# Kernel tuning notes

Hardware: AMD Instinct MI355X
Metric: run time of the kernel (lower is better)

## Reference

```python
import jax, jax.numpy as jnp
import numpy as np

B, S, H = 4, 128, 768
OUT, TAG = 24, 4


def setup_inputs() -> dict:
    key = jax.random.key(0)
    k1, k2, k3, k4, k5 = jax.random.split(key, 5)
    x = jax.random.normal(k1, (B, S, H), dtype=jnp.float32)
    # linear1: in 2H -> out 3H ; linear2: in 3H -> out TAG*OUT
    s1 = 1.0 / np.sqrt(2 * H)
    s2 = 1.0 / np.sqrt(3 * H)
    W1 = jax.random.uniform(k2, (2 * H, 3 * H), minval=-s1, maxval=s1, dtype=jnp.float32)
    b1 = jax.random.uniform(k3, (3 * H,), minval=-s1, maxval=s1, dtype=jnp.float32)
    W2 = jax.random.uniform(k4, (3 * H, TAG * OUT), minval=-s2, maxval=s2, dtype=jnp.float32)
    b2 = jax.random.uniform(k5, (TAG * OUT,), minval=-s2, maxval=s2, dtype=jnp.float32)
    return {"x": x, "W1": W1, "b1": b1, "W2": W2, "b2": b2}


def reference(x, W1, b1, W2, b2):
    b, s, h = x.shape
    # pairs[b,i,j] = concat(x[b,i], x[b,j]); avoid explicit 2H concat by
    # splitting W1 into head/tail halves (same math as cat -> linear1).
    W1h, W1t = W1[:h], W1[h:]
    head = jnp.einsum('bih,hk->bik', x, W1h)          # [B,S,3H]
    tail = jnp.einsum('bjh,hk->bjk', x, W1t)          # [B,S,3H]
    hid = head[:, :, None, :] + tail[:, None, :, :] + b1  # [B,S,S,3H]
    hid = jax.nn.relu(hid)  # dropout is identity in eval mode
    scores = jnp.einsum('bijk,ko->bijo', hid, W2) + b2     # [B,S,S,TAG*OUT]
    return scores.reshape(b, s, s, OUT, TAG)
```

## Files before the change

### kernel.cpp

```cpp
#include <hip/hip_runtime.h>
#include <hip/hip_bf16.h>


typedef __bf16 bf16x8 __attribute__((ext_vector_type(8)));
typedef _Float16 f16x8 __attribute__((ext_vector_type(8)));
typedef float f32x4 __attribute__((ext_vector_type(4)));

#define S_   128
#define H_   768
#define K3   2304
#define NOUT 96
#define NIT  36

__device__ __forceinline__ unsigned short f2bf(float f) {
    union { __bf16 b; unsigned short u; } c;
    c.b = (__bf16)f;
    return c.u;
}

__device__ __forceinline__ unsigned short f2h(float f) {
    union { _Float16 h; unsigned short u; } c;
    c.h = (_Float16)f;
    return c.u;
}

__device__ __forceinline__ void gload_lds16(const unsigned short* g, unsigned short* l) {
    __builtin_amdgcn_global_load_lds(
        (const __attribute__((address_space(1))) void*)g,
        (__attribute__((address_space(3))) void*)l,
        16, 0, 0);
}

__global__ __launch_bounds__(256) void k_prep(
        const float* __restrict__ x, unsigned short* __restrict__ xb,
        const float* __restrict__ W1, unsigned short* __restrict__ w1t,
        const float* __restrict__ W2, unsigned short* __restrict__ w2f) {
    __shared__ float tile[32][33];
    const int bid = blockIdx.x, tid = threadIdx.x;
    if (bid < 384) {
        int t = bid * 256 + tid;
        float4 v = ((const float4*)x)[t];
        ushort4 o;
        o.x = f2bf(v.x); o.y = f2bf(v.y); o.z = f2bf(v.z); o.w = f2bf(v.w);
        ((ushort4*)xb)[t] = o;
    } else if (bid < 3840) {
        int idx = bid - 384;
        int bx = idx % 72, by = (idx / 72) % 24, bz = idx / 1728;
        const float* src = W1 + (size_t)bz * H_ * K3;
        unsigned short* dst = w1t + (size_t)bz * K3 * H_;
        int c0 = bx * 32, r0 = by * 32;
        int row = tid >> 3, c4 = (tid & 7) * 4;
        float4 v = *(const float4*)(src + (size_t)(r0 + row) * K3 + c0 + c4);
        tile[row][c4 + 0] = v.x; tile[row][c4 + 1] = v.y;
        tile[row][c4 + 2] = v.z; tile[row][c4 + 3] = v.w;
        __syncthreads();
        ushort4 o;
        o.x = f2bf(tile[c4 + 0][row]); o.y = f2bf(tile[c4 + 1][row]);
        o.z = f2bf(tile[c4 + 2][row]); o.w = f2bf(tile[c4 + 3][row]);
        *(ushort4*)(dst + (size_t)(c0 + row) * H_ + r0 + c4) = o;
    } else {
        int t = (bid - 3840) * 256 + tid;
        int l = t & 63, f = (t >> 6) % 6, kc = t / 384;
        int k0 = kc * 32 + (l >> 4) * 8;
        int o  = f * 16 + (l & 15);
        unsigned short v[8];
#pragma unroll
        for (int e = 0; e < 8; e++)
            v[e] = f2h(W2[(size_t)(k0 + e) * NOUT + o]);
        *(uint4*)(w2f + (size_t)t * 8) = *(const uint4*)v;
    }
}

__global__ __launch_bounds__(256) void k_gemm1(
        const unsigned short* __restrict__ xb,
        const unsigned short* __restrict__ w1t,
        const float* __restrict__ b1,
        unsigned short* __restrict__ headh,
        unsigned short* __restrict__ tailsw) {
    __shared__ __align__(16) unsigned short AB[3][6144];
    const int tid = threadIdx.x;
    const int l = tid & 63, w = tid >> 6;
    const int m0 = blockIdx.y * 64;
    const int n0 = blockIdx.x * 128;
    const int wr = (w >> 1) * 32, wc = (w & 1) * 64;
    const int lr = l & 15, lk = (l >> 4) * 8;
    f32x4 acc[2][4] = {};
    const int NKT = H_ / 32;

    auto stage = [&](int sbuf, int kt) {
        {
            int row = tid >> 2, seg = (tid & 3) * 8;
            gload_lds16(xb + (size_t)(m0 + row) * H_ + kt * 32 + seg, &AB[sbuf][tid * 8]);
        }
#pragma unroll
        for (int p = 0; p < 2; ++p) {
            int idx = p * 256 + tid;
            int row = idx >> 2, seg = (idx & 3) * 8;
            gload_lds16(w1t + (size_t)(n0 + row) * H_ + kt * 32 + seg,
                        &AB[sbuf][2048 + idx * 8]);
        }
    };

    stage(0, 0);
    stage(1, 1);

    for (int n = 0; n < NKT; ++n) {
        asm volatile("s_waitcnt vmcnt(3)" ::: "memory");
        __builtin_amdgcn_s_barrier();
        stage((n + 2) % 3, (n + 2 < NKT) ? (n + 2) : (NKT - 1));

        const unsigned short* Ab = &AB[n % 3][0];
        const unsigned short* Bb = &AB[n % 3][2048];
        bf16x8 af[2], bfr[4];
#pragma unroll
        for (int i = 0; i < 2; i++) af[i]  = *(const bf16x8*)(Ab + (wr + i * 16 + lr) * 32 + lk);
#pragma unroll
        for (int j = 0; j < 4; j++) bfr[j] = *(const bf16x8*)(Bb + (wc + j * 16 + lr) * 32 + lk);
#pragma unroll
        for (int i = 0; i < 2; i++)
#pragma unroll
            for (int j = 0; j < 4; j++)
                acc[i][j] = __builtin_amdgcn_mfma_f32_16x16x32_bf16(af[i], bfr[j], acc[i][j], 0, 0, 0);
    }

    const bool tailblk = (n0 >= K3);
    const int nloc = n0 - (tailblk ? K3 : 0);
    const int lv = (l >> 4) * 4;
    if (!tailblk) {
#pragma unroll
        for (int j = 0; j < 4; j++) {
            int c = nloc + wc + j * 16 + lr;
#pragma unroll
            for (int i = 0; i < 2; i++) {
                int mrow = m0 + wr + i * 16 + lv;
#pragma unroll
                for (int e = 0; e < 4; e++)
                    headh[(size_t)(mrow + e) * K3 + c] = f2h(acc[i][j][e]);
            }
        }
    } else {
#pragma unroll
        for (int j = 0; j < 4; j++) {
            int c = nloc + wc + j * 16 + lr;
            float bias = b1[c];
            int chunk = c >> 6, kin = c & 63, u = kin >> 3, ee = kin & 7;
#pragma unroll
            for (int i = 0; i < 2; i++) {
                int mrow = m0 + wr + i * 16 + lv;
#pragma unroll
                for (int e = 0; e < 4; e++) {
                    int r = mrow + e;
                    int jbg = r >> 4, rr = r & 15;
                    size_t idx = (((size_t)(jbg * 36 + chunk) * 8 + u) * 16 + rr) * 8 + ee;
                    tailsw[idx] = f2h(acc[i][j][e] + bias);
                }
            }
        }
    }
}

__device__ __forceinline__ f16x8 form8t(uint4 hq, f16x8 t) {
    union { uint4 q; f16x8 v; } H;
    H.q = hq;
    f16x8 s = H.v + t;
    const f16x8 z = {0, 0, 0, 0, 0, 0, 0, 0};
    return __builtin_elementwise_max(s, z);
}

__global__ __launch_bounds__(256) void k_pair(
        const unsigned short* __restrict__ headh,
        const unsigned short* __restrict__ tailsw,
        const unsigned short* __restrict__ w2f,
        const float* __restrict__ b2,
        float* __restrict__ out) {
    __shared__ __align__(16) unsigned short wlds[4][6144];
    __shared__ __align__(16) unsigned short tlds[4][1024];

    const int tid = threadIdx.x;
    const int w = tid >> 6, l = tid & 63;
    const int lr = l & 15, lkq = l >> 4;
    const int lkoff = lkq * 8;
    const int jb = blockIdx.x;
    const int ig = blockIdx.y;
    const int b  = blockIdx.z;
    const int i0 = ig * 8;

    {
        int bid = jb + ig * 8 + b * 128;
        if ((bid >> 8) & 1) {
            __builtin_amdgcn_s_sleep(11);
            __builtin_amdgcn_s_sleep(11);
        }
    }

    const unsigned short* Hp   = headh + (size_t)(b * S_ + i0 + 2 * w) * K3;
    const unsigned short* Tsrc = tailsw + (size_t)(b * 8 + jb) * 36 * 1024;

    f32x4 acc[2][6] = {};
    float b2v[6];
#pragma unroll
    for (int f = 0; f < 6; f++) b2v[f] = b2[f * 16 + lr];

    auto stage = [&](int sbuf, int c) {
        const unsigned short* wsrc = w2f + (size_t)c * 6144;
#pragma unroll
        for (int i = 0; i < 3; ++i)
            gload_lds16(wsrc + i * 2048 + tid * 8, &wlds[sbuf][i * 2048 + tid * 8]);
        const unsigned short* tsrc = Tsrc + (size_t)c * 1024;
#pragma unroll
        for (int h = 0; h < 2; ++h)
            gload_lds16(tsrc + h * 512 + l * 8, &tlds[sbuf][h * 512 + l * 8]);
    };

    stage(0, 0);
    stage(1, 1);
    uint4 ha[2], hb[2];
#pragma unroll
    for (int kk = 0; kk < 2; kk++) {
        ha[kk] = *(const uint4*)(Hp + kk * 32 + lkoff);
        hb[kk] = *(const uint4*)(Hp + K3 + kk * 32 + lkoff);
    }

    for (int n = 0; n < NIT; ++n) {
        stage((n + 2) & 3, (n + 2 < NIT) ? (n + 2) : (NIT - 1));
        const int kn = ((n < NIT - 1) ? (n + 1) : n) * 64;
        uint4 han[2], hbn[2];
#pragma unroll
        for (int kk = 0; kk < 2; kk++) {
            han[kk] = *(const uint4*)(Hp + kn + kk * 32 + lkoff);
            hbn[kk] = *(const uint4*)(Hp + K3 + kn + kk * 32 + lkoff);
        }

        asm volatile("s_waitcnt vmcnt(9)" ::: "memory");
        __builtin_amdgcn_s_barrier();

        const unsigned short* Lb = &wlds[n & 3][0];
        const unsigned short* Tb = &tlds[n & 3][0];
        __builtin_amdgcn_s_setprio(1);
#pragma unroll
        for (int kk = 0; kk < 2; kk++) {
            f16x8 t8 = *(const f16x8*)(Tb + (kk * 4 + lkq) * 128 + lr * 8);
            f16x8 a0 = form8t(ha[kk], t8);
            f16x8 a1 = form8t(hb[kk], t8);
#pragma unroll
            for (int f = 0; f < 6; f++) {
                f16x8 bfr = *(const f16x8*)(Lb + kk * 3072 + f * 512 + l * 8);
                acc[0][f] = __builtin_amdgcn_mfma_f32_16x16x32_f16(a0, bfr, acc[0][f], 0, 0, 0);
                acc[1][f] = __builtin_amdgcn_mfma_f32_16x16x32_f16(a1, bfr, acc[1][f], 0, 0, 0);
            }
        }
        __builtin_amdgcn_s_setprio(0);
#pragma unroll
        for (int kk = 0; kk < 2; kk++) { ha[kk] = han[kk]; hb[kk] = hbn[kk]; }
    }

    float* O = out + (((size_t)(b * S_ + i0 + 2 * w)) * S_ + jb * 16) * NOUT;
#pragma unroll
    for (int q = 0; q < 2; q++)
#pragma unroll
        for (int f = 0; f < 6; f++)
#pragma unroll
            for (int e = 0; e < 4; e++) {
                int j = lkq * 4 + e;
                O[(size_t)q * S_ * NOUT + (size_t)j * NOUT + f * 16 + lr] = acc[q][f][e] + b2v[f];
            }
}

extern "C" void kernel_launch(void* const* d_in, const int* in_sizes, int n_in,
                              void* d_out, int out_size, void* d_ws, size_t ws_size,
                              hipStream_t stream) {
    const float* x  = (const float*)d_in[0];
    const float* W1 = (const float*)d_in[1];
    const float* b1 = (const float*)d_in[2];
    const float* W2 = (const float*)d_in[3];
    const float* b2 = (const float*)d_in[4];
    float* out = (float*)d_out;

    char* ws = (char*)d_ws;
    unsigned short* xb     = (unsigned short*)(ws);
    unsigned short* w1t    = (unsigned short*)(ws +   786432);
    unsigned short* w2f    = (unsigned short*)(ws +  7864320);
    unsigned short* headh  = (unsigned short*)(ws +  8306688);
    unsigned short* tailsw = (unsigned short*)(ws + 10665984);

    hipLaunchKernelGGL(k_prep, dim3(3948), dim3(256), 0, stream,
                       x, xb, W1, w1t, W2, w2f);
    hipLaunchKernelGGL(k_gemm1, dim3(36, 8), dim3(256), 0, stream,
                       xb, w1t, b1, headh, tailsw);
    hipLaunchKernelGGL(k_pair, dim3(8, 16, 4), dim3(256), 0, stream,
                       headh, tailsw, w2f, b2, out);
}
```

Measured before the change: 58.55 us.

## Switch pair kernel to 32x32 MFMA tiles with split-K across wave groups

Moves the pair kernel from 16x16x32 to 32x32x16 MFMA. The W2 and tail layouts written by the prep and gemm1 kernels change to match. Each block now covers 32 j-columns and 4 i-rows. Its two wave groups each handle half of the K range, and the partial sums are reduced through LDS at the end. Staging drops to a 3-buffer ring per group issued after the barrier, and the s_sleep staggering is removed. The aim is higher MFMA efficiency and more reuse per fragment, at the cost of an extra LDS reduction and half the waves idling during the epilogue.

```diff
diff --git a/kernel.cpp b/kernel.cpp
--- a/kernel.cpp
+++ b/kernel.cpp
@@ -5,12 +5,13 @@
 typedef __bf16 bf16x8 __attribute__((ext_vector_type(8)));
 typedef _Float16 f16x8 __attribute__((ext_vector_type(8)));
 typedef float f32x4 __attribute__((ext_vector_type(4)));
+typedef float f32x16 __attribute__((ext_vector_type(16)));
 
 #define S_   128
 #define H_   768
 #define K3   2304
 #define NOUT 96
-#define NIT  36
+#define NITG 36
 
 __device__ __forceinline__ unsigned short f2bf(float f) {
     union { __bf16 b; unsigned short u; } c;
@@ -60,9 +61,9 @@
         *(ushort4*)(dst + (size_t)(c0 + row) * H_ + r0 + c4) = o;
     } else {
         int t = (bid - 3840) * 256 + tid;
-        int l = t & 63, f = (t >> 6) % 6, kc = t / 384;
-        int k0 = kc * 32 + (l >> 4) * 8;
-        int o  = f * 16 + (l & 15);
+        int l = t & 63, og = (t >> 6) % 3, s = t / 192;
+        int k0 = s * 16 + (l >> 5) * 8;
+        int o  = og * 32 + (l & 31);
         unsigned short v[8];
 #pragma unroll
         for (int e = 0; e < 8; e++)
@@ -143,15 +144,15 @@
         for (int j = 0; j < 4; j++) {
             int c = nloc + wc + j * 16 + lr;
             float bias = b1[c];
-            int chunk = c >> 6, kin = c & 63, u = kin >> 3, ee = kin & 7;
+            int chunk = c >> 5, kin = c & 31, u = kin >> 3, ee = kin & 7;
 #pragma unroll
             for (int i = 0; i < 2; i++) {
                 int mrow = m0 + wr + i * 16 + lv;
 #pragma unroll
                 for (int e = 0; e < 4; e++) {
                     int r = mrow + e;
-                    int jbg = r >> 4, rr = r & 15;
-                    size_t idx = (((size_t)(jbg * 36 + chunk) * 8 + u) * 16 + rr) * 8 + ee;
+                    int jbg = r >> 5, rr = r & 31;
+                    size_t idx = (((size_t)(jbg * 72 + chunk) * 4 + u) * 32 + rr) * 8 + ee;
                     tailsw[idx] = f2h(acc[i][j][e] + bias);
                 }
             }
@@ -173,97 +174,125 @@
         const unsigned short* __restrict__ w2f,
         const float* __restrict__ b2,
         float* __restrict__ out) {
-    __shared__ __align__(16) unsigned short wlds[4][6144];
-    __shared__ __align__(16) unsigned short tlds[4][1024];
+    __shared__ __align__(16) unsigned short smem[24576];
 
     const int tid = threadIdx.x;
     const int w = tid >> 6, l = tid & 63;
-    const int lr = l & 15, lkq = l >> 4;
-    const int lkoff = lkq * 8;
+    const int g  = w >> 1;
+    const int wi = w & 1;
+    const int p  = w & 1;
+    const int lo = l & 31;
+    const int kq = l >> 5;
+    const int ko = kq * 8;
     const int jb = blockIdx.x;
     const int ig = blockIdx.y;
     const int b  = blockIdx.z;
-    const int i0 = ig * 8;
-
-    {
-        int bid = jb + ig * 8 + b * 128;
-        if ((bid >> 8) & 1) {
-            __builtin_amdgcn_s_sleep(11);
-            __builtin_amdgcn_s_sleep(11);
-        }
-    }
-
-    const unsigned short* Hp   = headh + (size_t)(b * S_ + i0 + 2 * w) * K3;
-    const unsigned short* Tsrc = tailsw + (size_t)(b * 8 + jb) * 36 * 1024;
-
-    f32x4 acc[2][6] = {};
-    float b2v[6];
-#pragma unroll
-    for (int f = 0; f < 6; f++) b2v[f] = b2[f * 16 + lr];
-
-    auto stage = [&](int sbuf, int c) {
-        const unsigned short* wsrc = w2f + (size_t)c * 6144;
+    const int i0 = ig * 4 + wi * 2;
+    const int cbase = g * NITG;
+
+    const unsigned short* Hp   = headh + (size_t)(b * S_ + i0) * K3;
+    const unsigned short* Tsrc = tailsw + (size_t)(b * 4 + jb) * 72 * 1024;
+
+    f32x16 acc[2][3] = {};
+
+    auto stage = [&](int sbuf, int n) {
+        const int cc = g * NITG + n;
+        const unsigned short* wsrc = w2f + (size_t)cc * 3072;
+        unsigned short* wdst = &smem[(g * 3 + sbuf) * 3072];
 #pragma unroll
         for (int i = 0; i < 3; ++i)
-            gload_lds16(wsrc + i * 2048 + tid * 8, &wlds[sbuf][i * 2048 + tid * 8]);
-        const unsigned short* tsrc = Tsrc + (size_t)c * 1024;
-#pragma unroll
-        for (int h = 0; h < 2; ++h)
-            gload_lds16(tsrc + h * 512 + l * 8, &tlds[sbuf][h * 512 + l * 8]);
+            gload_lds16(wsrc + (p * 3 + i) * 512 + l * 8, wdst + (p * 3 + i) * 512 + l * 8);
+        const unsigned short* tsrc = Tsrc + (size_t)cc * 1024;
+        unsigned short* tdst = &smem[18432 + (g * 3 + sbuf) * 1024];
+        gload_lds16(tsrc + p * 512 + l * 8, tdst + p * 512 + l * 8);
     };
 
     stage(0, 0);
     stage(1, 1);
-    uint4 ha[2], hb[2];
-#pragma unroll
-    for (int kk = 0; kk < 2; kk++) {
-        ha[kk] = *(const uint4*)(Hp + kk * 32 + lkoff);
-        hb[kk] = *(const uint4*)(Hp + K3 + kk * 32 + lkoff);
-    }
-
-    for (int n = 0; n < NIT; ++n) {
-        stage((n + 2) & 3, (n + 2 < NIT) ? (n + 2) : (NIT - 1));
-        const int kn = ((n < NIT - 1) ? (n + 1) : n) * 64;
-        uint4 han[2], hbn[2];
-#pragma unroll
-        for (int kk = 0; kk < 2; kk++) {
-            han[kk] = *(const uint4*)(Hp + kn + kk * 32 + lkoff);
-            hbn[kk] = *(const uint4*)(Hp + K3 + kn + kk * 32 + lkoff);
-        }
-
-        asm volatile("s_waitcnt vmcnt(9)" ::: "memory");
+    uint4 hc[2][2], hn[2][2];
+#pragma unroll
+    for (int si = 0; si < 2; si++) {
+        const int kb = cbase * 32 + si * 16 + ko;
+        hc[0][si] = *(const uint4*)(Hp + kb);
+        hc[1][si] = *(const uint4*)(Hp + K3 + kb);
+    }
+
+    for (int n = 0; n < NITG; ++n) {
+        const int cn = (n < NITG - 1) ? n + 1 : n;
+        const int kbn = (cbase + cn) * 32;
+#pragma unroll
+        for (int si = 0; si < 2; si++) {
+            hn[0][si] = *(const uint4*)(Hp + kbn + si * 16 + ko);
+            hn[1][si] = *(const uint4*)(Hp + K3 + kbn + si * 16 + ko);
+        }
+
+        asm volatile("s_waitcnt vmcnt(12)" ::: "memory");
         __builtin_amdgcn_s_barrier();
 
-        const unsigned short* Lb = &wlds[n & 3][0];
-        const unsigned short* Tb = &tlds[n & 3][0];
+        stage((n + 2) % 3, (n + 2 < NITG) ? (n + 2) : (NITG - 1));
+
+        const unsigned short* Lb = &smem[(g * 3 + n % 3) * 3072];
+        const unsigned short* Tb = &smem[18432 + (g * 3 + n % 3) * 1024];
         __builtin_amdgcn_s_setprio(1);
 #pragma unroll
-        for (int kk = 0; kk < 2; kk++) {
-            f16x8 t8 = *(const f16x8*)(Tb + (kk * 4 + lkq) * 128 + lr * 8);
-            f16x8 a0 = form8t(ha[kk], t8);
-            f16x8 a1 = form8t(hb[kk], t8);
-#pragma unroll
-            for (int f = 0; f < 6; f++) {
-                f16x8 bfr = *(const f16x8*)(Lb + kk * 3072 + f * 512 + l * 8);
-                acc[0][f] = __builtin_amdgcn_mfma_f32_16x16x32_f16(a0, bfr, acc[0][f], 0, 0, 0);
-                acc[1][f] = __builtin_amdgcn_mfma_f32_16x16x32_f16(a1, bfr, acc[1][f], 0, 0, 0);
+        for (int si = 0; si < 2; si++) {
+            f16x8 t8 = *(const f16x8*)(Tb + ((si * 2 + kq) * 32 + lo) * 8);
+            f16x8 a0 = form8t(hc[0][si], t8);
+            f16x8 a1 = form8t(hc[1][si], t8);
+#pragma unroll
+            for (int og = 0; og < 3; og++) {
+                f16x8 bfr = *(const f16x8*)(Lb + ((si * 3 + og) * 64 + l) * 8);
+                acc[0][og] = __builtin_amdgcn_mfma_f32_32x32x16_f16(a0, bfr, acc[0][og], 0, 0, 0);
+                acc[1][og] = __builtin_amdgcn_mfma_f32_32x32x16_f16(a1, bfr, acc[1][og], 0, 0, 0);
             }
         }
         __builtin_amdgcn_s_setprio(0);
 #pragma unroll
-        for (int kk = 0; kk < 2; kk++) { ha[kk] = han[kk]; hb[kk] = hbn[kk]; }
-    }
-
-    float* O = out + (((size_t)(b * S_ + i0 + 2 * w)) * S_ + jb * 16) * NOUT;
-#pragma unroll
-    for (int q = 0; q < 2; q++)
-#pragma unroll
-        for (int f = 0; f < 6; f++)
-#pragma unroll
-            for (int e = 0; e < 4; e++) {
-                int j = lkq * 4 + e;
-                O[(size_t)q * S_ * NOUT + (size_t)j * NOUT + f * 16 + lr] = acc[q][f][e] + b2v[f];
-            }
+        for (int si = 0; si < 2; si++) { hc[0][si] = hn[0][si]; hc[1][si] = hn[1][si]; }
+    }
+
+    asm volatile("s_waitcnt vmcnt(0)" ::: "memory");
+    __syncthreads();
+    float4* red = (float4*)&smem[0];
+    const int lid = wi * 64 + l;
+    if (g == 1) {
+#pragma unroll
+        for (int qi = 0; qi < 2; qi++)
+#pragma unroll
+            for (int og = 0; og < 3; og++)
+#pragma unroll
+                for (int pp = 0; pp < 4; pp++)
+                    red[((qi * 3 + og) * 4 + pp) * 128 + lid] =
+                        make_float4(acc[qi][og][pp * 4 + 0], acc[qi][og][pp * 4 + 1],
+                                    acc[qi][og][pp * 4 + 2], acc[qi][og][pp * 4 + 3]);
+    }
+    __syncthreads();
+    if (g == 0) {
+        float b2v[3];
+#pragma unroll
+        for (int og = 0; og < 3; og++) b2v[og] = b2[og * 32 + lo];
+#pragma unroll
+        for (int qi = 0; qi < 2; qi++)
+#pragma unroll
+            for (int og = 0; og < 3; og++)
+#pragma unroll
+                for (int pp = 0; pp < 4; pp++) {
+                    float4 v = red[((qi * 3 + og) * 4 + pp) * 128 + lid];
+                    acc[qi][og][pp * 4 + 0] += v.x; acc[qi][og][pp * 4 + 1] += v.y;
+                    acc[qi][og][pp * 4 + 2] += v.z; acc[qi][og][pp * 4 + 3] += v.w;
+                }
+#pragma unroll
+        for (int qi = 0; qi < 2; qi++) {
+            float* O = out + ((size_t)(b * S_ + i0 + qi) * S_ + jb * 32) * NOUT + lo;
+#pragma unroll
+            for (int og = 0; og < 3; og++)
+#pragma unroll
+                for (int r = 0; r < 16; r++) {
+                    int j = (r & 3) + 8 * (r >> 2) + 4 * kq;
+                    O[(size_t)j * NOUT + og * 32] = acc[qi][og][r] + b2v[og];
+                }
+        }
+    }
 }
 
 extern "C" void kernel_launch(void* const* d_in, const int* in_sizes, int n_in,
@@ -287,6 +316,6 @@
                        x, xb, W1, w1t, W2, w2f);
     hipLaunchKernelGGL(k_gemm1, dim3(36, 8), dim3(256), 0, stream,
                        xb, w1t, b1, headh, tailsw);
-    hipLaunchKernelGGL(k_pair, dim3(8, 16, 4), dim3(256), 0, stream,
+    hipLaunchKernelGGL(k_pair, dim3(4, 32, 4), dim3(256), 0, stream,
                        headh, tailsw, w2f, b2, out);
 }
```

Result: slower. 62.35 us (+6.5%).

## Split W1 transpose into 64x64-tile kernel and halve gemm1 N-tile

Applied to the files above, without the earlier changes.

Moves the W1 transpose/bf16 conversion into its own kernel that uses 64x64 LDS tiles with four float4 loads per thread instead of 32x32 tiles. The x and W2 conversions stay in a separate smaller prep kernel. The gemm1 tile shrinks from 64x128 to 64x64, doubling the grid to 576 blocks to fill more CUs on the 256-CU device. The cost is one extra kernel launch, less operand reuse per block in gemm1, and a larger LDS footprint in the transpose kernel.

```diff
diff --git a/kernel.cpp b/kernel.cpp
--- a/kernel.cpp
+++ b/kernel.cpp
@@ -31,11 +31,9 @@
         16, 0, 0);
 }
 
-__global__ __launch_bounds__(256) void k_prep(
+__global__ __launch_bounds__(256) void k_prep_xw2(
         const float* __restrict__ x, unsigned short* __restrict__ xb,
-        const float* __restrict__ W1, unsigned short* __restrict__ w1t,
         const float* __restrict__ W2, unsigned short* __restrict__ w2f) {
-    __shared__ float tile[32][33];
     const int bid = blockIdx.x, tid = threadIdx.x;
     if (bid < 384) {
         int t = bid * 256 + tid;
@@ -43,23 +41,8 @@
         ushort4 o;
         o.x = f2bf(v.x); o.y = f2bf(v.y); o.z = f2bf(v.z); o.w = f2bf(v.w);
         ((ushort4*)xb)[t] = o;
-    } else if (bid < 3840) {
-        int idx = bid - 384;
-        int bx = idx % 72, by = (idx / 72) % 24, bz = idx / 1728;
-        const float* src = W1 + (size_t)bz * H_ * K3;
-        unsigned short* dst = w1t + (size_t)bz * K3 * H_;
-        int c0 = bx * 32, r0 = by * 32;
-        int row = tid >> 3, c4 = (tid & 7) * 4;
-        float4 v = *(const float4*)(src + (size_t)(r0 + row) * K3 + c0 + c4);
-        tile[row][c4 + 0] = v.x; tile[row][c4 + 1] = v.y;
-        tile[row][c4 + 2] = v.z; tile[row][c4 + 3] = v.w;
-        __syncthreads();
-        ushort4 o;
-        o.x = f2bf(tile[c4 + 0][row]); o.y = f2bf(tile[c4 + 1][row]);
-        o.z = f2bf(tile[c4 + 2][row]); o.w = f2bf(tile[c4 + 3][row]);
-        *(ushort4*)(dst + (size_t)(c0 + row) * H_ + r0 + c4) = o;
     } else {
-        int t = (bid - 3840) * 256 + tid;
+        int t = (bid - 384) * 256 + tid;
         int l = t & 63, f = (t >> 6) % 6, kc = t / 384;
         int k0 = kc * 32 + (l >> 4) * 8;
         int o  = f * 16 + (l & 15);
@@ -68,6 +51,32 @@
         for (int e = 0; e < 8; e++)
             v[e] = f2h(W2[(size_t)(k0 + e) * NOUT + o]);
         *(uint4*)(w2f + (size_t)t * 8) = *(const uint4*)v;
+    }
+}
+
+__global__ __launch_bounds__(256) void k_prep_w1(
+        const float* __restrict__ W1, unsigned short* __restrict__ w1t) {
+    __shared__ float tile[64][65];
+    const int idx = blockIdx.x, tid = threadIdx.x;
+    int bx = idx % 36, by = (idx / 36) % 12, bz = idx / 432;
+    const float* src = W1 + (size_t)bz * H_ * K3;
+    unsigned short* dst = w1t + (size_t)bz * K3 * H_;
+    int c0 = bx * 64, r0 = by * 64;
+    int row = tid >> 2, cs = (tid & 3) * 16;
+#pragma unroll
+    for (int i = 0; i < 4; i++) {
+        float4 v = *(const float4*)(src + (size_t)(r0 + row) * K3 + c0 + cs + i * 4);
+        tile[row][cs + i * 4 + 0] = v.x; tile[row][cs + i * 4 + 1] = v.y;
+        tile[row][cs + i * 4 + 2] = v.z; tile[row][cs + i * 4 + 3] = v.w;
+    }
+    __syncthreads();
+    int c = tid >> 2, rs = (tid & 3) * 16;
+#pragma unroll
+    for (int i = 0; i < 4; i++) {
+        ushort4 o;
+        o.x = f2bf(tile[rs + i * 4 + 0][c]); o.y = f2bf(tile[rs + i * 4 + 1][c]);
+        o.z = f2bf(tile[rs + i * 4 + 2][c]); o.w = f2bf(tile[rs + i * 4 + 3][c]);
+        *(ushort4*)(dst + (size_t)(c0 + c) * H_ + r0 + rs + i * 4) = o;
     }
 }
 
@@ -77,49 +86,41 @@
         const float* __restrict__ b1,
         unsigned short* __restrict__ headh,
         unsigned short* __restrict__ tailsw) {
-    __shared__ __align__(16) unsigned short AB[3][6144];
+    __shared__ __align__(16) unsigned short AB[3][4096];
     const int tid = threadIdx.x;
     const int l = tid & 63, w = tid >> 6;
     const int m0 = blockIdx.y * 64;
-    const int n0 = blockIdx.x * 128;
-    const int wr = (w >> 1) * 32, wc = (w & 1) * 64;
+    const int n0 = blockIdx.x * 64;
+    const int wr = (w >> 1) * 32, wc = (w & 1) * 32;
     const int lr = l & 15, lk = (l >> 4) * 8;
-    f32x4 acc[2][4] = {};
+    f32x4 acc[2][2] = {};
     const int NKT = H_ / 32;
 
     auto stage = [&](int sbuf, int kt) {
-        {
-            int row = tid >> 2, seg = (tid & 3) * 8;
-            gload_lds16(xb + (size_t)(m0 + row) * H_ + kt * 32 + seg, &AB[sbuf][tid * 8]);
-        }
-#pragma unroll
-        for (int p = 0; p < 2; ++p) {
-            int idx = p * 256 + tid;
-            int row = idx >> 2, seg = (idx & 3) * 8;
-            gload_lds16(w1t + (size_t)(n0 + row) * H_ + kt * 32 + seg,
-                        &AB[sbuf][2048 + idx * 8]);
-        }
+        int row = tid >> 2, seg = (tid & 3) * 8;
+        gload_lds16(xb  + (size_t)(m0 + row) * H_ + kt * 32 + seg, &AB[sbuf][tid * 8]);
+        gload_lds16(w1t + (size_t)(n0 + row) * H_ + kt * 32 + seg, &AB[sbuf][2048 + tid * 8]);
     };
 
     stage(0, 0);
     stage(1, 1);
 
     for (int n = 0; n < NKT; ++n) {
-        asm volatile("s_waitcnt vmcnt(3)" ::: "memory");
+        asm volatile("s_waitcnt vmcnt(2)" ::: "memory");
         __builtin_amdgcn_s_barrier();
         stage((n + 2) % 3, (n + 2 < NKT) ? (n + 2) : (NKT - 1));
 
         const unsigned short* Ab = &AB[n % 3][0];
         const unsigned short* Bb = &AB[n % 3][2048];
-        bf16x8 af[2], bfr[4];
+        bf16x8 af[2], bfr[2];
 #pragma unroll
         for (int i = 0; i < 2; i++) af[i]  = *(const bf16x8*)(Ab + (wr + i * 16 + lr) * 32 + lk);
 #pragma unroll
-        for (int j = 0; j < 4; j++) bfr[j] = *(const bf16x8*)(Bb + (wc + j * 16 + lr) * 32 + lk);
+        for (int j = 0; j < 2; j++) bfr[j] = *(const bf16x8*)(Bb + (wc + j * 16 + lr) * 32 + lk);
 #pragma unroll
         for (int i = 0; i < 2; i++)
 #pragma unroll
-            for (int j = 0; j < 4; j++)
+            for (int j = 0; j < 2; j++)
                 acc[i][j] = __builtin_amdgcn_mfma_f32_16x16x32_bf16(af[i], bfr[j], acc[i][j], 0, 0, 0);
     }
 
@@ -128,7 +129,7 @@
     const int lv = (l >> 4) * 4;
     if (!tailblk) {
 #pragma unroll
-        for (int j = 0; j < 4; j++) {
+        for (int j = 0; j < 2; j++) {
             int c = nloc + wc + j * 16 + lr;
 #pragma unroll
             for (int i = 0; i < 2; i++) {
@@ -140,7 +141,7 @@
         }
     } else {
 #pragma unroll
-        for (int j = 0; j < 4; j++) {
+        for (int j = 0; j < 2; j++) {
             int c = nloc + wc + j * 16 + lr;
             float bias = b1[c];
             int chunk = c >> 6, kin = c & 63, u = kin >> 3, ee = kin & 7;
@@ -283,9 +284,9 @@
     unsigned short* headh  = (unsigned short*)(ws +  8306688);
     unsigned short* tailsw = (unsigned short*)(ws + 10665984);
 
-    hipLaunchKernelGGL(k_prep, dim3(3948), dim3(256), 0, stream,
-                       x, xb, W1, w1t, W2, w2f);
-    hipLaunchKernelGGL(k_gemm1, dim3(36, 8), dim3(256), 0, stream,
+    hipLaunchKernelGGL(k_prep_w1, dim3(864), dim3(256), 0, stream, W1, w1t);
+    hipLaunchKernelGGL(k_prep_xw2, dim3(492), dim3(256), 0, stream, x, xb, W2, w2f);
+    hipLaunchKernelGGL(k_gemm1, dim3(72, 8), dim3(256), 0, stream,
                        xb, w1t, b1, headh, tailsw);
     hipLaunchKernelGGL(k_pair, dim3(8, 16, 4), dim3(256), 0, stream,
                        headh, tailsw, w2f, b2, out);
```

Result: slower. 61.14 us (+4.4%).

## Process two K-steps per barrier in pair kernel and drop sleep stagger

Applied to the files above, without the earlier changes.

Unrolls the main K loop by two so each barrier-guarded step stages two LDS buffers (n+2, n+3) and runs MFMAs for two K-chunks. Head-row register prefetches are reorganised to match, with adjusted vmcnt waits between the two compute halves. This halves the number of workgroup barriers and gives the loads more time to overlap with compute. It also removes the s_sleep stagger applied to half the blocks. The trade-offs are higher register pressure from the extra prefetched operands and the loss of whatever contention relief the stagger provided.

```diff
diff --git a/kernel.cpp b/kernel.cpp
--- a/kernel.cpp
+++ b/kernel.cpp
@@ -11,6 +11,7 @@
 #define K3   2304
 #define NOUT 96
 #define NIT  36
+#define NSI  18
 
 __device__ __forceinline__ unsigned short f2bf(float f) {
     union { __bf16 b; unsigned short u; } c;
@@ -185,14 +186,6 @@
     const int b  = blockIdx.z;
     const int i0 = ig * 8;
 
-    {
-        int bid = jb + ig * 8 + b * 128;
-        if ((bid >> 8) & 1) {
-            __builtin_amdgcn_s_sleep(11);
-            __builtin_amdgcn_s_sleep(11);
-        }
-    }
-
     const unsigned short* Hp   = headh + (size_t)(b * S_ + i0 + 2 * w) * K3;
     const unsigned short* Tsrc = tailsw + (size_t)(b * 8 + jb) * 36 * 1024;
 
@@ -221,37 +214,75 @@
         hb[kk] = *(const uint4*)(Hp + K3 + kk * 32 + lkoff);
     }
 
-    for (int n = 0; n < NIT; ++n) {
+    for (int m = 0; m < NSI; ++m) {
+        const int n = 2 * m;
+        uint4 hao[2], hbo[2];
+        {
+            const int kb = (n + 1) * 64;
+#pragma unroll
+            for (int kk = 0; kk < 2; kk++) {
+                hao[kk] = *(const uint4*)(Hp + kb + kk * 32 + lkoff);
+                hbo[kk] = *(const uint4*)(Hp + K3 + kb + kk * 32 + lkoff);
+            }
+        }
+        uint4 hae[2], hbe[2];
+        {
+            const int kb = ((n + 2 < NIT) ? (n + 2) : (NIT - 1)) * 64;
+#pragma unroll
+            for (int kk = 0; kk < 2; kk++) {
+                hae[kk] = *(const uint4*)(Hp + kb + kk * 32 + lkoff);
+                hbe[kk] = *(const uint4*)(Hp + K3 + kb + kk * 32 + lkoff);
+            }
+        }
+
+        asm volatile("s_waitcnt vmcnt(8)" ::: "memory");
+        __builtin_amdgcn_s_barrier();
+
         stage((n + 2) & 3, (n + 2 < NIT) ? (n + 2) : (NIT - 1));
-        const int kn = ((n < NIT - 1) ? (n + 1) : n) * 64;
-        uint4 han[2], hbn[2];
-#pragma unroll
-        for (int kk = 0; kk < 2; kk++) {
-            han[kk] = *(const uint4*)(Hp + kn + kk * 32 + lkoff);
-            hbn[kk] = *(const uint4*)(Hp + K3 + kn + kk * 32 + lkoff);
-        }
-
-        asm volatile("s_waitcnt vmcnt(9)" ::: "memory");
-        __builtin_amdgcn_s_barrier();
-
-        const unsigned short* Lb = &wlds[n & 3][0];
-        const unsigned short* Tb = &tlds[n & 3][0];
-        __builtin_amdgcn_s_setprio(1);
-#pragma unroll
-        for (int kk = 0; kk < 2; kk++) {
-            f16x8 t8 = *(const f16x8*)(Tb + (kk * 4 + lkq) * 128 + lr * 8);
-            f16x8 a0 = form8t(ha[kk], t8);
-            f16x8 a1 = form8t(hb[kk], t8);
-#pragma unroll
-            for (int f = 0; f < 6; f++) {
-                f16x8 bfr = *(const f16x8*)(Lb + kk * 3072 + f * 512 + l * 8);
-                acc[0][f] = __builtin_amdgcn_mfma_f32_16x16x32_f16(a0, bfr, acc[0][f], 0, 0, 0);
-                acc[1][f] = __builtin_amdgcn_mfma_f32_16x16x32_f16(a1, bfr, acc[1][f], 0, 0, 0);
-            }
-        }
-        __builtin_amdgcn_s_setprio(0);
-#pragma unroll
-        for (int kk = 0; kk < 2; kk++) { ha[kk] = han[kk]; hb[kk] = hbn[kk]; }
+        stage((n + 3) & 3, (n + 3 < NIT) ? (n + 3) : (NIT - 1));
+
+        {
+            const unsigned short* Lb = &wlds[n & 3][0];
+            const unsigned short* Tb = &tlds[n & 3][0];
+            __builtin_amdgcn_s_setprio(1);
+#pragma unroll
+            for (int kk = 0; kk < 2; kk++) {
+                f16x8 t8 = *(const f16x8*)(Tb + (kk * 4 + lkq) * 128 + lr * 8);
+                f16x8 a0 = form8t(ha[kk], t8);
+                f16x8 a1 = form8t(hb[kk], t8);
+#pragma unroll
+                for (int f = 0; f < 6; f++) {
+                    f16x8 bfr = *(const f16x8*)(Lb + kk * 3072 + f * 512 + l * 8);
+                    acc[0][f] = __builtin_amdgcn_mfma_f32_16x16x32_f16(a0, bfr, acc[0][f], 0, 0, 0);
+                    acc[1][f] = __builtin_amdgcn_mfma_f32_16x16x32_f16(a1, bfr, acc[1][f], 0, 0, 0);
+                }
+            }
+            __builtin_amdgcn_s_setprio(0);
+        }
+
+        asm volatile("s_waitcnt vmcnt(14)" ::: "memory");
+
+        {
+            const unsigned short* Lb = &wlds[(n + 1) & 3][0];
+            const unsigned short* Tb = &tlds[(n + 1) & 3][0];
+            __builtin_amdgcn_s_setprio(1);
+#pragma unroll
+            for (int kk = 0; kk < 2; kk++) {
+                f16x8 t8 = *(const f16x8*)(Tb + (kk * 4 + lkq) * 128 + lr * 8);
+                f16x8 a0 = form8t(hao[kk], t8);
+                f16x8 a1 = form8t(hbo[kk], t8);
+#pragma unroll
+                for (int f = 0; f < 6; f++) {
+                    f16x8 bfr = *(const f16x8*)(Lb + kk * 3072 + f * 512 + l * 8);
+                    acc[0][f] = __builtin_amdgcn_mfma_f32_16x16x32_f16(a0, bfr, acc[0][f], 0, 0, 0);
+                    acc[1][f] = __builtin_amdgcn_mfma_f32_16x16x32_f16(a1, bfr, acc[1][f], 0, 0, 0);
+                }
+            }
+            __builtin_amdgcn_s_setprio(0);
+        }
+
+#pragma unroll
+        for (int kk = 0; kk < 2; kk++) { ha[kk] = hae[kk]; hb[kk] = hbe[kk]; }
     }
 
     float* O = out + (((size_t)(b * S_ + i0 + 2 * w)) * S_ + jb * 16) * NOUT;
```

Result: faster. 55.83 us (-4.7%).
